# Kernel optimization log

Hardware: AMD Instinct MI355X
Metric: run time of the kernel (lower is better)

Reference implementation:

```python
import jax, jax.numpy as jnp
import numpy as np

B, N, D_IN, D_OUT, L, T = 8, 512, 1024, 1024, 16, 4096


def setup_inputs() -> dict:
    key = jax.random.key(0)
    k1, k2, k3 = jax.random.split(key, 3)
    pooled_vectors = jax.random.normal(k1, (B, N, D_IN), dtype=jnp.float32)
    # stacked nn.Linear weights, each (out, in), bias=False
    W = jax.random.normal(k2, (L, D_OUT, D_IN), dtype=jnp.float32) * 0.02
    pooling_indices = jnp.sort(jax.random.randint(k3, (N,), 0, T, dtype=jnp.int64))
    return {
        "pooled_vectors": pooled_vectors,
        "W": W,
        "pooling_indices": pooling_indices,
        "target_length": T,
    }


def reference(pooled_vectors, W, pooling_indices, target_length):
    # pooled_vectors: (B, N, D_in); W: (L, D_out, D_in); pooling_indices: (N,) sorted
    Bn, Nn, _ = pooled_vectors.shape
    Ln = W.shape[0]
    t = jnp.arange(target_length)
    # segment i covers [start_i, idx_i + 1); searchsorted finds the covering segment
    seg = jnp.searchsorted(pooling_indices, t, side="left")  # (T,)
    valid = seg < Nn  # positions past the last pooling index stay zero
    segc = jnp.clip(seg, 0, Nn - 1)
    start = jnp.where(segc > 0, pooling_indices[segc - 1] + 1, 0)
    lidx = jnp.minimum(t - start, Ln - 1)  # position-specific linear index, capped
    # apply all L position linears to every pooled vector: (B, N, L, D_out)
    trans = jnp.einsum("bnd,lod->bnlo", pooled_vectors, W)
    out = trans[:, segc, lidx]  # gather per output position -> (B, T, D_out)
    return jnp.where(valid[None, :, None], out, jnp.zeros((), out.dtype))
```

## Files before the change

### kernel.cpp

```cpp
#include <hip/hip_runtime.h>
#include <stdint.h>

#define B_    8
#define N_    512
#define DIN   1024
#define DOUT  1024
#define L_    16
#define T_    4096

#define BM 128
#define BN 128
#define BK 32
#define NB (DOUT / BN)
#define NKT (DIN / BK)
#define MT_MAX 288
#define ZROW ((long)B_ * N_)

typedef __attribute__((ext_vector_type(8))) short short8;
typedef __attribute__((ext_vector_type(4))) float f32x4;

#define POOLED_ELEMS ((long)B_ * N_ * DIN + DIN)
#define WS_W_OFF     ((size_t)POOLED_ELEMS * 2)
#define WS_META_OFF  (WS_W_OFF + (size_t)L_ * DOUT * DIN * 2)

__device__ __forceinline__ unsigned short f2bf(float f) {
  unsigned u = __float_as_uint(f);
  u += 0x7FFFu + ((u >> 16) & 1u);
  return (unsigned short)(u >> 16);
}

__device__ __forceinline__ void gload_lds16(const void* g, void* l) {
  __builtin_amdgcn_global_load_lds(
      (const __attribute__((address_space(1))) void*)g,
      (__attribute__((address_space(3))) void*)l, 16, 0, 0);
}

__global__ void k_convert(const float* __restrict__ pooled,
                          const float* __restrict__ W,
                          unsigned short* __restrict__ wsP,
                          unsigned short* __restrict__ wsW2) {
  const long np4 = (long)B_ * N_ * DIN / 4;
  const long nz4 = DIN / 4;
  const long nwu = (long)L_ * 64 * 32 * 64;
  long i = (long)blockIdx.x * blockDim.x + threadIdx.x;
  const long stride = (long)gridDim.x * blockDim.x;
  for (; i < np4 + nz4 + nwu; i += stride) {
    if (i < np4) {
      float4 v = ((const float4*)pooled)[i];
      ushort4 o = { f2bf(v.x), f2bf(v.y), f2bf(v.z), f2bf(v.w) };
      ((ushort4*)wsP)[i] = o;
    } else if (i < np4 + nz4) {
      ushort4 z = {0, 0, 0, 0};
      ((ushort4*)wsP)[i] = z;
    } else {
      long u = i - np4 - nz4;
      int ln = (int)(u & 63); long tmp = u >> 6;
      int kb = (int)(tmp & 31); tmp >>= 5;
      int cb = (int)(tmp & 63); int l = (int)(tmp >> 6);
      int r = cb * 16 + (ln & 15);
      int k = kb * 32 + (ln >> 4) * 8;
      const float* src = W + ((long)l * DOUT + r) * DIN + k;
      float4 v0 = *(const float4*)(src);
      float4 v1 = *(const float4*)(src + 4);
      ushort4 o0 = { f2bf(v0.x), f2bf(v0.y), f2bf(v0.z), f2bf(v0.w) };
      ushort4 o1 = { f2bf(v1.x), f2bf(v1.y), f2bf(v1.z), f2bf(v1.w) };
      ((ushort4*)wsW2)[u * 2]     = o0;
      ((ushort4*)wsW2)[u * 2 + 1] = o1;
    }
  }
}

__global__ void k_prep(const int* __restrict__ pidx,
                       unsigned* __restrict__ tlist,
                       int* __restrict__ goff, int* __restrict__ grows,
                       unsigned* __restrict__ table, int* __restrict__ ntiles) {
  __shared__ int sp[N_];
  __shared__ int cnt[L_], pos[L_];
  const int tid = threadIdx.x;
  if (tid < N_) sp[tid] = pidx[tid];
  if (tid < L_) cnt[tid] = 0;
  __syncthreads();

  int start = tid ? sp[tid - 1] + 1 : 0;
  int len = sp[tid] - start + 1;
  if (len < 0) len = 0;
  const int nfull = len < 15 ? len : 15;

  for (int l2 = 0; l2 < nfull; ++l2) atomicAdd(&cnt[l2], 1);
  if (len > 15) atomicAdd(&cnt[15], (len - 15 + 254) / 255);
  if (tid == N_ - 1) {
    int invlen = T_ - 1 - sp[N_ - 1];
    if (invlen > 0) atomicAdd(&cnt[15], (invlen + 254) / 255);
  }
  __syncthreads();
  if (tid == 0) {
    int off = 0;
    for (int l2 = 0; l2 < L_; ++l2) {
      pos[l2] = off; goff[l2] = off; grows[l2] = cnt[l2] * B_;
      off += cnt[l2];
    }
  }
  __syncthreads();

  for (int l2 = 0; l2 < nfull; ++l2) {
    int p = atomicAdd(&pos[l2], 1);
    tlist[p] = (unsigned)(start + l2) | ((unsigned)tid << 12) | (1u << 22);
  }
  if (len > 15) {
    int rem = len - 15, tt2 = start + 15;
    while (rem > 0) {
      int rr = rem > 255 ? 255 : rem;
      int p = atomicAdd(&pos[15], 1);
      tlist[p] = (unsigned)tt2 | ((unsigned)tid << 12) | ((unsigned)rr << 22);
      tt2 += rr; rem -= rr;
    }
  }
  if (tid == N_ - 1) {
    int tt2 = sp[N_ - 1] + 1;
    int rem = T_ - tt2;
    while (rem > 0) {
      int rr = rem > 255 ? 255 : rem;
      int p = atomicAdd(&pos[15], 1);
      tlist[p] = (unsigned)tt2 | (1023u << 12) | ((unsigned)rr << 22);
      tt2 += rr; rem -= rr;
    }
  }
  __syncthreads();
  if (tid == 0) {
    int tt = 0;
    for (int l2 = 0; l2 < L_; ++l2) {
      int rows = cnt[l2] * B_;
      for (int r0 = 0; r0 < rows; r0 += BM) table[tt++] = (unsigned)l2 | ((unsigned)r0 << 4);
    }
    *ntiles = tt;
  }
}

__global__ __launch_bounds__(256, 3)
void k_gemm(const unsigned short* __restrict__ wsP,
            const unsigned short* __restrict__ wsW2,
            const unsigned* __restrict__ tlist,
            const int* __restrict__ goff,
            const int* __restrict__ grows,
            const unsigned* __restrict__ table,
            const int* __restrict__ ntiles,
            float* __restrict__ out) {
  const int bid = blockIdx.x;
  const int mt = bid >> 3;
  const int nt = bid & 7;
  if (mt >= *ntiles) return;

  const unsigned te = table[mt];
  const int l    = te & 15;
  const int row0 = (int)(te >> 4);
  const int toff = goff[l];
  const int rows = grows[l];

  __shared__ __align__(16) unsigned short As[2][BM * BK];
  __shared__ __align__(16) float escr[4][16 * 68];

  const int tid  = threadIdx.x;
  const int lane = tid & 63;
  const int w    = tid >> 6;
  const int wm   = w >> 1;
  const int wn   = w & 1;

  const int srow = tid >> 2;
  const int sx4  = ((tid & 3) ^ ((srow >> 1) & 3)) * 16;
  const char* aptr0;
  const char* aptr1;
  {
    long re[2];
#pragma unroll
    for (int r = 0; r < 2; ++r) {
      int rg = row0 + r * 64 + srow;
      if (rg < rows) {
        unsigned e = tlist[toff + (rg >> 3)];
        unsigned n = (e >> 12) & 0x3FF;
        int b = rg & 7;
        re[r] = (n >= N_) ? ZROW * (long)DIN
                          : ((long)(b * N_ + (int)n)) * DIN;
      } else re[r] = ZROW * (long)DIN;
    }
    aptr0 = (const char*)(wsP + re[0]) + sx4;
    aptr1 = (const char*)(wsP + re[1]) + sx4;
  }

#define STG_A(t_, sb) do { \
  gload_lds16(aptr0 + (t_) * 64, (char*)As[sb] + w * 1024); \
  gload_lds16(aptr1 + (t_) * 64, (char*)As[sb] + 4096 + w * 1024); } while (0)

  const int arow = wm * 64 + (lane & 15);
  const int axr  = ((lane >> 4) ^ (((lane & 15) >> 1) & 3)) * 16;

  const unsigned short* wbase =
      wsW2 + (((long)l * 64 + nt * 8 + wn * 4) * 32) * 512 + lane * 8;
#define LDB(dst, t_) do { _Pragma("unroll") \
  for (int n_ = 0; n_ < 4; ++n_) \
    dst[n_] = *(const short8*)(wbase + n_ * (32 * 512) + (t_) * 512); } while (0)

#define DSA(bb) do { _Pragma("unroll") \
  for (int m_ = 0; m_ < 4; ++m_) \
    af[m_] = *(const short8*)((const char*)As[bb] + (arow + m_ * 16) * 64 + axr); } while (0)

#define MM(BF) do { \
  __builtin_amdgcn_s_setprio(1); \
  _Pragma("unroll") for (int n_ = 0; n_ < 4; ++n_) \
    _Pragma("unroll") for (int m_ = 0; m_ < 4; ++m_) \
      acc[m_][n_] = __builtin_amdgcn_mfma_f32_16x16x32_bf16(af[m_], BF[n_], acc[m_][n_], 0, 0, 0); \
  __builtin_amdgcn_s_setprio(0); } while (0)

  f32x4 acc[4][4];
#pragma unroll
  for (int m = 0; m < 4; ++m)
#pragma unroll
    for (int n = 0; n < 4; ++n)
      acc[m][n] = (f32x4){0.f, 0.f, 0.f, 0.f};

  short8 af[4], bf_a[4], bf_b[4];

  STG_A(0, 0);
  LDB(bf_a, 0);
  __syncthreads();

#pragma unroll
  for (int j = 0; j < NKT / 2; ++j) {
    const int t0 = 2 * j, t1 = 2 * j + 1;
    STG_A(t1, 1);
    LDB(bf_b, t1);
    DSA(0);
    MM(bf_a);
    __syncthreads();
    if (t0 + 2 < NKT) { STG_A(t0 + 2, 0); LDB(bf_a, t0 + 2); }
    DSA(1);
    MM(bf_b);
    __syncthreads();
  }

  {
    float* sc = escr[w];
#pragma unroll
    for (int m = 0; m < 4; ++m) {
#pragma unroll
      for (int n = 0; n < 4; ++n)
#pragma unroll
        for (int jj = 0; jj < 4; ++jj)
          sc[((lane >> 4) * 4 + jj) * 68 + n * 16 + (lane & 15)] = acc[m][n][jj];
      asm volatile("s_waitcnt lgkmcnt(0)" ::: "memory");
#pragma unroll
      for (int r0 = 0; r0 < 16; r0 += 4) {
        int rtl = r0 + (lane >> 4);
        float4 v = *(const float4*)(sc + rtl * 68 + (lane & 15) * 4);
        int rg = row0 + wm * 64 + m * 16 + rtl;
        if (rg < rows) {
          unsigned e = tlist[toff + (rg >> 3)];
          int b = rg & 7;
          int tt = (int)(e & 0xFFFu);
          int rep = (int)(e >> 22);
          float* p = out + ((long)b * T_ + tt) * DOUT + nt * BN + wn * 64 + (lane & 15) * 4;
          for (int r = 0; r < rep; ++r) { *(float4*)p = v; p += DOUT; }
        }
      }
      asm volatile("s_waitcnt lgkmcnt(0)" ::: "memory");
    }
  }
#undef STG_A
#undef LDB
#undef DSA
#undef MM
}

extern "C" void kernel_launch(void* const* d_in, const int* in_sizes, int n_in,
                              void* d_out, int out_size, void* d_ws, size_t ws_size,
                              hipStream_t stream) {
  const float* pooled = (const float*)d_in[0];
  const float* W      = (const float*)d_in[1];
  const int*   pidx   = (const int*)d_in[2];
  float* out = (float*)d_out;

  char* ws = (char*)d_ws;
  unsigned short* wsP  = (unsigned short*)(ws);
  unsigned short* wsW2 = (unsigned short*)(ws + WS_W_OFF);
  int* meta  = (int*)(ws + WS_META_OFF);
  unsigned* tlist = (unsigned*)meta;
  int* goff  = meta + 8 * T_;
  int* grows = meta + 8 * T_ + 16;
  unsigned* table = (unsigned*)(meta + 8 * T_ + 32);
  int* ntiles = meta + 8 * T_ + 32 + MT_MAX;

  k_prep<<<1, 512, 0, stream>>>(pidx, tlist, goff, grows, table, ntiles);
  k_convert<<<2048, 256, 0, stream>>>(pooled, W, wsP, wsW2);
  k_gemm<<<MT_MAX * NB, 256, 0, stream>>>(wsP, wsW2, tlist, goff, grows, table,
                                          ntiles, out);
}
```

Measured before the change: 127.6 us.

## Restructure grouped GEMM into persistent per-wave independent 64x64 tiles

Replaces the 128x128 block tile, where four waves cooperate through barriers, with 64x64 tiles that each wave computes on its own using private LDS buffers. A persistent grid of 512 blocks loops over the M-tiles, and synchronisation uses explicit vmcnt/lgkmcnt waits instead of __syncthreads. The epilogue scratch reuses the A buffers, which frees LDS and raises the occupancy target to 4. The aim is to cut barrier stalls and tail imbalance, at the cost of less A/B reuse per tile, since each wave reloads B per tile and A traffic across column tiles doubles.

```diff
diff --git a/kernel.cpp b/kernel.cpp
--- a/kernel.cpp
+++ b/kernel.cpp
@@ -8,12 +8,8 @@
 #define L_    16
 #define T_    4096
 
-#define BM 128
-#define BN 128
-#define BK 32
-#define NB (DOUT / BN)
-#define NKT (DIN / BK)
-#define MT_MAX 288
+#define NKT (DIN / 32)
+#define MT_MAX 544
 #define ZROW ((long)B_ * N_)
 
 typedef __attribute__((ext_vector_type(8))) short short8;
@@ -130,13 +126,13 @@
     int tt = 0;
     for (int l2 = 0; l2 < L_; ++l2) {
       int rows = cnt[l2] * B_;
-      for (int r0 = 0; r0 < rows; r0 += BM) table[tt++] = (unsigned)l2 | ((unsigned)r0 << 4);
+      for (int r0 = 0; r0 < rows; r0 += 64) table[tt++] = (unsigned)l2 | ((unsigned)r0 << 4);
     }
     *ntiles = tt;
   }
 }
 
-__global__ __launch_bounds__(256, 3)
+__global__ __launch_bounds__(256, 4)
 void k_gemm(const unsigned short* __restrict__ wsP,
             const unsigned short* __restrict__ wsW2,
             const unsigned* __restrict__ tlist,
@@ -145,129 +141,114 @@
             const unsigned* __restrict__ table,
             const int* __restrict__ ntiles,
             float* __restrict__ out) {
-  const int bid = blockIdx.x;
-  const int mt = bid >> 3;
-  const int nt = bid & 7;
-  if (mt >= *ntiles) return;
-
-  const unsigned te = table[mt];
-  const int l    = te & 15;
-  const int row0 = (int)(te >> 4);
-  const int toff = goff[l];
-  const int rows = grows[l];
-
-  __shared__ __align__(16) unsigned short As[2][BM * BK];
-  __shared__ __align__(16) float escr[4][16 * 68];
-
   const int tid  = threadIdx.x;
   const int lane = tid & 63;
   const int w    = tid >> 6;
-  const int wm   = w >> 1;
-  const int wn   = w & 1;
-
-  const int srow = tid >> 2;
-  const int sx4  = ((tid & 3) ^ ((srow >> 1) & 3)) * 16;
-  const char* aptr0;
-  const char* aptr1;
-  {
-    long re[2];
-#pragma unroll
-    for (int r = 0; r < 2; ++r) {
-      int rg = row0 + r * 64 + srow;
+  const int ct   = blockIdx.x & 15;
+  const int q    = blockIdx.x >> 4;
+  const int NTM  = *ntiles;
+
+  __shared__ __align__(16) unsigned short As[4][2][64 * 32];
+
+  const int sx4 = ((lane & 3) ^ (((lane >> 2) >> 1) & 3)) * 16;
+  const int arow = lane & 15;
+  const int axr  = ((lane >> 4) ^ (((lane & 15) >> 1) & 3)) * 16;
+
+#define STG(t_, bb) do { _Pragma("unroll") \
+  for (int i_ = 0; i_ < 4; ++i_) \
+    gload_lds16(aptr[i_] + (t_) * 64, (char*)As[w][bb] + i_ * 1024); } while (0)
+#define LDB(t_) do { _Pragma("unroll") \
+  for (int n_ = 0; n_ < 4; ++n_) \
+    bf[n_] = *(const short8*)(wbase + n_ * (32 * 512) + (t_) * 512); } while (0)
+#define DSA(bb) do { _Pragma("unroll") \
+  for (int m_ = 0; m_ < 4; ++m_) \
+    af[m_] = *(const short8*)((const char*)As[w][bb] + (arow + m_ * 16) * 64 + axr); } while (0)
+#define VM(n_) asm volatile("s_waitcnt vmcnt(" #n_ ")" ::: "memory")
+#define LGKM0  asm volatile("s_waitcnt lgkmcnt(0)" ::: "memory")
+#define MMX do { _Pragma("unroll") for (int n_ = 0; n_ < 4; ++n_) \
+  _Pragma("unroll") for (int m_ = 0; m_ < 4; ++m_) \
+    acc[m_][n_] = __builtin_amdgcn_mfma_f32_16x16x32_bf16(af[m_], bf[n_], acc[m_][n_], 0, 0, 0); } while (0)
+
+  for (int mtl = q * 4 + w; mtl < NTM; mtl += 128) {
+    const unsigned te = table[mtl];
+    const int l    = te & 15;
+    const int row0 = (int)(te >> 4);
+    const int toff = goff[l];
+    const int rows = grows[l];
+
+    const char* aptr[4];
+#pragma unroll
+    for (int i = 0; i < 4; ++i) {
+      int rg = row0 + i * 16 + (lane >> 2);
+      long re;
       if (rg < rows) {
         unsigned e = tlist[toff + (rg >> 3)];
         unsigned n = (e >> 12) & 0x3FF;
         int b = rg & 7;
-        re[r] = (n >= N_) ? ZROW * (long)DIN
-                          : ((long)(b * N_ + (int)n)) * DIN;
-      } else re[r] = ZROW * (long)DIN;
-    }
-    aptr0 = (const char*)(wsP + re[0]) + sx4;
-    aptr1 = (const char*)(wsP + re[1]) + sx4;
-  }
-
-#define STG_A(t_, sb) do { \
-  gload_lds16(aptr0 + (t_) * 64, (char*)As[sb] + w * 1024); \
-  gload_lds16(aptr1 + (t_) * 64, (char*)As[sb] + 4096 + w * 1024); } while (0)
-
-  const int arow = wm * 64 + (lane & 15);
-  const int axr  = ((lane >> 4) ^ (((lane & 15) >> 1) & 3)) * 16;
-
-  const unsigned short* wbase =
-      wsW2 + (((long)l * 64 + nt * 8 + wn * 4) * 32) * 512 + lane * 8;
-#define LDB(dst, t_) do { _Pragma("unroll") \
-  for (int n_ = 0; n_ < 4; ++n_) \
-    dst[n_] = *(const short8*)(wbase + n_ * (32 * 512) + (t_) * 512); } while (0)
-
-#define DSA(bb) do { _Pragma("unroll") \
-  for (int m_ = 0; m_ < 4; ++m_) \
-    af[m_] = *(const short8*)((const char*)As[bb] + (arow + m_ * 16) * 64 + axr); } while (0)
-
-#define MM(BF) do { \
-  __builtin_amdgcn_s_setprio(1); \
-  _Pragma("unroll") for (int n_ = 0; n_ < 4; ++n_) \
-    _Pragma("unroll") for (int m_ = 0; m_ < 4; ++m_) \
-      acc[m_][n_] = __builtin_amdgcn_mfma_f32_16x16x32_bf16(af[m_], BF[n_], acc[m_][n_], 0, 0, 0); \
-  __builtin_amdgcn_s_setprio(0); } while (0)
-
-  f32x4 acc[4][4];
-#pragma unroll
-  for (int m = 0; m < 4; ++m)
-#pragma unroll
-    for (int n = 0; n < 4; ++n)
-      acc[m][n] = (f32x4){0.f, 0.f, 0.f, 0.f};
-
-  short8 af[4], bf_a[4], bf_b[4];
-
-  STG_A(0, 0);
-  LDB(bf_a, 0);
-  __syncthreads();
-
-#pragma unroll
-  for (int j = 0; j < NKT / 2; ++j) {
-    const int t0 = 2 * j, t1 = 2 * j + 1;
-    STG_A(t1, 1);
-    LDB(bf_b, t1);
-    DSA(0);
-    MM(bf_a);
-    __syncthreads();
-    if (t0 + 2 < NKT) { STG_A(t0 + 2, 0); LDB(bf_a, t0 + 2); }
-    DSA(1);
-    MM(bf_b);
-    __syncthreads();
-  }
-
-  {
-    float* sc = escr[w];
-#pragma unroll
-    for (int m = 0; m < 4; ++m) {
+        re = (n >= N_) ? ZROW * (long)DIN : ((long)(b * N_ + (int)n)) * DIN;
+      } else re = ZROW * (long)DIN;
+      aptr[i] = (const char*)(wsP + re) + sx4;
+    }
+    const unsigned short* wbase =
+        wsW2 + (((long)l * 64 + ct * 4) * 32) * 512 + lane * 8;
+
+    f32x4 acc[4][4];
+#pragma unroll
+    for (int m = 0; m < 4; ++m)
 #pragma unroll
       for (int n = 0; n < 4; ++n)
-#pragma unroll
-        for (int jj = 0; jj < 4; ++jj)
-          sc[((lane >> 4) * 4 + jj) * 68 + n * 16 + (lane & 15)] = acc[m][n][jj];
-      asm volatile("s_waitcnt lgkmcnt(0)" ::: "memory");
-#pragma unroll
-      for (int r0 = 0; r0 < 16; r0 += 4) {
-        int rtl = r0 + (lane >> 4);
-        float4 v = *(const float4*)(sc + rtl * 68 + (lane & 15) * 4);
-        int rg = row0 + wm * 64 + m * 16 + rtl;
-        if (rg < rows) {
-          unsigned e = tlist[toff + (rg >> 3)];
-          int b = rg & 7;
-          int tt = (int)(e & 0xFFFu);
-          int rep = (int)(e >> 22);
-          float* p = out + ((long)b * T_ + tt) * DOUT + nt * BN + wn * 64 + (lane & 15) * 4;
-          for (int r = 0; r < rep; ++r) { *(float4*)p = v; p += DOUT; }
+        acc[m][n] = (f32x4){0.f, 0.f, 0.f, 0.f};
+
+    short8 af[4], bf[4];
+
+    STG(0, 0);
+#pragma unroll
+    for (int j = 0; j < NKT / 2; ++j) {
+      const int t0 = 2 * j, t1 = 2 * j + 1;
+      LDB(t0);
+      STG(t1, 1);
+      VM(4);
+      DSA(0); LGKM0; MMX;
+      LDB(t1);
+      if (t1 + 1 < NKT) { STG(t1 + 1, 0); VM(4); }
+      else              { VM(0); }
+      DSA(1); LGKM0; MMX;
+    }
+
+    {
+      float* sc = (float*)As[w];
+#pragma unroll
+      for (int m = 0; m < 4; ++m) {
+#pragma unroll
+        for (int n = 0; n < 4; ++n)
+#pragma unroll
+          for (int jj = 0; jj < 4; ++jj)
+            sc[((lane >> 4) * 4 + jj) * 68 + n * 16 + (lane & 15)] = acc[m][n][jj];
+        LGKM0;
+#pragma unroll
+        for (int r0 = 0; r0 < 16; r0 += 4) {
+          int rtl = r0 + (lane >> 4);
+          float4 v = *(const float4*)(sc + rtl * 68 + (lane & 15) * 4);
+          int rg = row0 + m * 16 + rtl;
+          if (rg < rows) {
+            unsigned e = tlist[toff + (rg >> 3)];
+            int b = rg & 7;
+            int tt = (int)(e & 0xFFFu);
+            int rep = (int)(e >> 22);
+            float* p = out + ((long)b * T_ + tt) * DOUT + ct * 64 + (lane & 15) * 4;
+            for (int r = 0; r < rep; ++r) { *(float4*)p = v; p += DOUT; }
+          }
         }
+        LGKM0;
       }
-      asm volatile("s_waitcnt lgkmcnt(0)" ::: "memory");
-    }
-  }
-#undef STG_A
+    }
+  }
+#undef STG
 #undef LDB
 #undef DSA
-#undef MM
+#undef VM
+#undef LGKM0
+#undef MMX
 }
 
 extern "C" void kernel_launch(void* const* d_in, const int* in_sizes, int n_in,
@@ -290,6 +271,6 @@
 
   k_prep<<<1, 512, 0, stream>>>(pidx, tlist, goff, grows, table, ntiles);
   k_convert<<<2048, 256, 0, stream>>>(pooled, W, wsP, wsW2);
-  k_gemm<<<MT_MAX * NB, 256, 0, stream>>>(wsP, wsW2, tlist, goff, grows, table,
-                                          ntiles, out);
-}
+  k_gemm<<<512, 256, 0, stream>>>(wsP, wsW2, tlist, goff, grows, table,
+                                  ntiles, out);
+}
```

Result: slower. 207.5 us (+62.6%).
